# Kernel optimization log

Measured on AMD Instinct MI355X. Metric: run time of the kernel, lower is better.

Reference implementation:

```python
import jax, jax.numpy as jnp
import numpy as np

# Model constants (from source: model_dim=1024, head_dim=128, num_heads=8)
L = 8          # num layers (reduced from 16 for tractable reference memory)
T = 2048       # packed tokens, B == 1 (varlen)
DIM = 1024
NH = 8
NKV = 4        # GQA kv heads
HD = 128
KVD = NKV * HD
BLOCK = 128
WS = 3
WIN = WS * BLOCK           # sliding-window size for 'S' layers
ATTN_SCALE = 0.12
PATTERN = 'SSSL'
GATE_CH = 32
EPS = 1.1920929e-07        # torch F.rms_norm default eps = finfo(fp32).eps


def rms_norm(x):
    return x * jax.lax.rsqrt(jnp.mean(x * x, axis=-1, keepdims=True) + EPS)


def apply_rotary(x, cos, sin):
    # x: [T, H, HD]; cos/sin: [T, 1, HD//2]
    d = x.shape[-1] // 2
    x1, x2 = x[..., :d], x[..., d:]
    return jnp.concatenate([x1 * cos + x2 * sin, -x1 * sin + x2 * cos], axis=-1)


def has_ve(layer_idx, n_layer):
    return layer_idx % 2 == (n_layer - 1) % 2


def setup_inputs() -> dict:
    key = jax.random.key(0)
    ks = jax.random.split(key, 9)
    x = jax.random.normal(ks[0], (1, T, DIM), jnp.float32)
    ve = jax.random.normal(ks[1], (L, T, KVD), jnp.float32)
    s = DIM ** -0.5
    Wq = jax.random.normal(ks[2], (L, DIM, NH * HD), jnp.float32) * s
    Wk = jax.random.normal(ks[3], (L, DIM, KVD), jnp.float32) * s
    Wv = jax.random.normal(ks[4], (L, DIM, KVD), jnp.float32) * s
    Wo = jax.random.normal(ks[5], (L, NH * HD, DIM), jnp.float32) * (NH * HD) ** -0.5
    Wgate = jax.random.normal(ks[6], (L, GATE_CH, NKV), jnp.float32) * GATE_CH ** -0.5
    Wfc = jax.random.normal(ks[7], (L, DIM, 4 * DIM), jnp.float32) * s
    Wproj = jax.random.normal(ks[8], (L, 4 * DIM, DIM), jnp.float32) * (4 * DIM) ** -0.5
    # RoPE tables (absolute positions of the packed batch, as in the source)
    inv_freq = 1.0 / (10000.0 ** (jnp.arange(HD // 2, dtype=jnp.float32) / (HD // 2)))
    ang = jnp.arange(T, dtype=jnp.float32)[:, None] * inv_freq[None, :]
    cos = jnp.cos(ang)[:, None, :]
    sin = jnp.sin(ang)[:, None, :]
    # cu_seqlens: 4 packed documents of 512 tokens
    seqlens = jnp.array([0, 512, 1024, 1536, 2048], dtype=jnp.int32)
    return dict(x=x, ve=ve, Wq=Wq, Wk=Wk, Wv=Wv, Wo=Wo, Wgate=Wgate,
                Wfc=Wfc, Wproj=Wproj, cos=cos, sin=sin, seqlens=seqlens)


def reference(x, ve, Wq, Wk, Wv, Wo, Wgate, Wfc, Wproj, cos, sin, seqlens):
    h = x[0]  # [T, DIM], B == 1 (varlen packing)
    pos = jnp.arange(T)
    doc = jnp.searchsorted(seqlens, pos, side='right') - 1
    diff = pos[:, None] - pos[None, :]
    base = (diff >= 0) & (doc[:, None] == doc[None, :])   # causal within doc
    mask_S = base & (diff <= WIN)                         # sliding window
    neg = jnp.float32(-1e30)
    rep = NH // NKV
    for l in range(L):
        xn = rms_norm(h)
        q = (xn @ Wq[l]).reshape(T, NH, HD)
        k = (xn @ Wk[l]).reshape(T, NKV, HD)
        v = (xn @ Wv[l]).reshape(T, NKV, HD)
        if has_ve(l, L):
            gate = 2.0 * jax.nn.sigmoid(xn[:, :GATE_CH] @ Wgate[l])  # [T, NKV]
            v = v + gate[:, :, None] * ve[l].reshape(T, NKV, HD)
        q = rms_norm(apply_rotary(q, cos, sin))
        k = rms_norm(apply_rotary(k, cos, sin))
        k = jnp.repeat(k, rep, axis=1)   # GQA -> full heads
        v2 = jnp.repeat(v, rep, axis=1)
        scores = jnp.einsum('thd,shd->hts', q, k) * ATTN_SCALE  # [NH, T, T]
        mask = mask_S if PATTERN[l % len(PATTERN)] == 'S' else base
        scores = jnp.where(mask[None], scores, neg)
        p = jax.nn.softmax(scores, axis=-1)
        y = jnp.einsum('hts,shd->thd', p, v2).reshape(T, NH * HD)
        h = h + y @ Wo[l]
        m = jnp.square(jax.nn.relu(rms_norm(h) @ Wfc[l]))  # relu(x)^2 MLP
        h = h + m @ Wproj[l]
    return h[None]
```

## Files before the change

kernel.cpp:

```cpp
#include <hip/hip_runtime.h>
#include <hip/hip_bf16.h>
#include <cstdint>
#include <cstddef>

#define TT     2048
#define DMODEL 1024
#define NHQ    8
#define HD     128
#define KVD    512
#define WIN    384
#define EPSF   1.1920929e-07f
#define SCALE  0.12f

typedef __attribute__((ext_vector_type(8))) short bf16x8;
typedef __attribute__((ext_vector_type(4))) float f32x4;

#define WAITV(N)  asm volatile("s_waitcnt vmcnt(" #N ")" ::: "memory")

__device__ __forceinline__ float b2f(unsigned short u) {
    unsigned int i = ((unsigned int)u) << 16; float f; __builtin_memcpy(&f, &i, 4); return f;
}
__device__ __forceinline__ unsigned short f2b(float f) {
    unsigned int i; __builtin_memcpy(&i, &f, 4);
    unsigned int r = (i + 0x7fffu + ((i >> 16) & 1u)) >> 16;
    return (unsigned short)r;
}

__device__ __forceinline__ void gl_lds16(const unsigned short* g, unsigned short* l) {
    __builtin_amdgcn_global_load_lds(
        (const __attribute__((address_space(1))) unsigned int*)g,
        (__attribute__((address_space(3))) unsigned int*)l, 16, 0, 0);
}

__global__ __launch_bounds__(256)
void convT_k(const float* __restrict__ Wq, const float* __restrict__ Wk,
             const float* __restrict__ Wv, const float* __restrict__ Wo,
             const float* __restrict__ Wfc, const float* __restrict__ Wproj,
             unsigned short* __restrict__ Bqkv, unsigned short* __restrict__ Bo,
             unsigned short* __restrict__ Bfc, unsigned short* __restrict__ Bproj)
{
    __shared__ float lt[64][65];
    const int bid = blockIdx.x, tid = threadIdx.x, l = blockIdx.y;

    const float* W; unsigned short* Wt; int K, N, t, nbase;
    if (bid < 256)        { W = Wq    + (size_t)l * 1024 * 1024; Wt = Bqkv  + (size_t)l * 2048 * 1024; K = 1024; N = 1024; t = bid;        nbase = 0;    }
    else if (bid < 384)   { W = Wk    + (size_t)l * 1024 * 512;  Wt = Bqkv  + (size_t)l * 2048 * 1024; K = 1024; N = 512;  t = bid - 256;  nbase = 1024; }
    else if (bid < 512)   { W = Wv    + (size_t)l * 1024 * 512;  Wt = Bqkv  + (size_t)l * 2048 * 1024; K = 1024; N = 512;  t = bid - 384;  nbase = 1536; }
    else if (bid < 768)   { W = Wo    + (size_t)l * 1024 * 1024; Wt = Bo    + (size_t)l * 1024 * 1024; K = 1024; N = 1024; t = bid - 512;  nbase = 0;    }
    else if (bid < 1792)  { W = Wfc   + (size_t)l * 1024 * 4096; Wt = Bfc   + (size_t)l * 4096 * 1024; K = 1024; N = 4096; t = bid - 768;  nbase = 0;    }
    else                  { W = Wproj + (size_t)l * 4096 * 1024; Wt = Bproj + (size_t)l * 1024 * 4096; K = 4096; N = 1024; t = bid - 1792; nbase = 0;    }

    const int ktiles = K >> 6;
    const int k0 = (t % ktiles) * 64, n0 = (t / ktiles) * 64;

    #pragma unroll
    for (int i = 0; i < 4; ++i) {
        int k = (tid >> 4) + i * 16;
        int col4 = (tid & 15) * 4;
        float4 v = *(const float4*)(W + (size_t)(k0 + k) * N + n0 + col4);
        lt[col4 + 0][k] = v.x;
        lt[col4 + 1][k] = v.y;
        lt[col4 + 2][k] = v.z;
        lt[col4 + 3][k] = v.w;
    }
    __syncthreads();
    #pragma unroll
    for (int i = 0; i < 2; ++i) {
        int idx = tid + i * 256;
        int n = idx >> 3, kc = (idx & 7) * 8;
        unsigned short o[8];
        #pragma unroll
        for (int j = 0; j < 8; ++j) o[j] = f2b(lt[n][kc + j]);
        *(uint4*)(Wt + (size_t)(nbase + n0 + n) * K + k0 + kc) = *(const uint4*)o;
    }
}

template<int EPI>
__global__ __launch_bounds__(256, 2)
void gemm4(const unsigned short* __restrict__ A, const unsigned short* __restrict__ Bt,
           float* __restrict__ Cf, unsigned short* __restrict__ Cb,
           int K, int ksplit, int Ntot)
{
    __shared__ unsigned short As[2 * 128 * 64];
    __shared__ unsigned short Bs[2 * 128 * 64];
    const int BUF = 128 * 64;
    const int tid = threadIdx.x, lane = tid & 63, wv = tid >> 6;

    const int gx = gridDim.x;
    const int nwg = gx * gridDim.y;
    const int ihw = blockIdx.y * gx + blockIdx.x;
    const int q = nwg >> 3, r = nwg & 7;
    const int xcd = ihw & 7, pos = ihw >> 3;
    const int lg = (xcd < r) ? xcd * (q + 1) + pos
                             : r * (q + 1) + (xcd - r) * q + pos;
    const int m0 = (lg % gx) * 128, n0 = (lg / gx) * 128;

    const int kbeg = blockIdx.z * ksplit;
    const int NT = ksplit >> 6;

    const int wr = (wv >> 1) * 64, wc = (wv & 1) * 64;
    const int l15 = lane & 15, g = lane >> 4;
    const int srow = lane >> 3;
    const int sxor = (((lane & 7) ^ srow) << 3);

    const unsigned short* gA0 = A  + (size_t)(m0 + wv * 32 + srow) * K + sxor;
    const unsigned short* gB0 = Bt + (size_t)(n0 + wv * 32 + srow) * K + sxor;

    auto stage = [&](int t) {
        const int b = t & 1;
        const size_t k = (size_t)kbeg + ((size_t)t << 6);
        unsigned short* la = As + b * BUF + (wv * 32) * 64;
        unsigned short* lb = Bs + b * BUF + (wv * 32) * 64;
        #pragma unroll
        for (int c = 0; c < 4; ++c) {
            gl_lds16(gA0 + (size_t)(c * 8) * K + k, la + c * 8 * 64);
            gl_lds16(gB0 + (size_t)(c * 8) * K + k, lb + c * 8 * 64);
        }
    };

    f32x4 acc[4][4] = {};

    stage(0);
    for (int t = 0; t < NT; ++t) {
        if (t + 1 < NT) { stage(t + 1); WAITV(8); }
        else            { WAITV(0); }
        __builtin_amdgcn_s_barrier();

        const unsigned short* Ac = As + (t & 1) * BUF;
        const unsigned short* Bc = Bs + (t & 1) * BUF;
        bf16x8 af[4][2], bfv[4][2];
        #pragma unroll
        for (int mi = 0; mi < 4; ++mi) {
            const int row = wr + mi * 16 + l15, x = row & 7;
            #pragma unroll
            for (int kk = 0; kk < 2; ++kk)
                af[mi][kk] = *(const bf16x8*)(Ac + row * 64 + (((kk * 4 + g) ^ x) << 3));
        }
        #pragma unroll
        for (int ni = 0; ni < 4; ++ni) {
            const int row = wc + ni * 16 + l15, x = row & 7;
            #pragma unroll
            for (int kk = 0; kk < 2; ++kk)
                bfv[ni][kk] = *(const bf16x8*)(Bc + row * 64 + (((kk * 4 + g) ^ x) << 3));
        }
        __builtin_amdgcn_s_setprio(1);
        #pragma unroll
        for (int kk = 0; kk < 2; ++kk)
            #pragma unroll
            for (int mi = 0; mi < 4; ++mi)
                #pragma unroll
                for (int ni = 0; ni < 4; ++ni)
                    acc[mi][ni] = __builtin_amdgcn_mfma_f32_16x16x32_bf16(af[mi][kk], bfv[ni][kk], acc[mi][ni], 0, 0, 0);
        __builtin_amdgcn_s_setprio(0);
        __builtin_amdgcn_s_barrier();
    }

    const int lr4 = (lane >> 4) * 4;
    float* Cz = Cf + (size_t)blockIdx.z * TT * Ntot;
    #pragma unroll
    for (int mi = 0; mi < 4; ++mi)
        #pragma unroll
        for (int ni = 0; ni < 4; ++ni)
            #pragma unroll
            for (int r2 = 0; r2 < 4; ++r2) {
                int row = m0 + wr + mi * 16 + lr4 + r2;
                int col = n0 + wc + ni * 16 + l15;
                size_t idx = (size_t)row * Ntot + col;
                float v = acc[mi][ni][r2];
                if (EPI == 0) Cz[idx] = v;
                else {
                    float z = v > 0.f ? v * v : 0.f;
                    Cb[idx] = f2b(z);
                }
            }
}

__global__ __launch_bounds__(256)
void rmsnormF_k(float* __restrict__ h, const float* __restrict__ part, int nz,
                unsigned short* __restrict__ xn)
{
    const int t = blockIdx.x, tid = threadIdx.x;
    const size_t idx = (size_t)t * (DMODEL / 4) + tid;
    float4 v = ((const float4*)h)[idx];
    for (int z = 0; z < nz; ++z) {
        float4 p = ((const float4*)part)[idx + (size_t)z * (TT * DMODEL / 4)];
        v.x += p.x; v.y += p.y; v.z += p.z; v.w += p.w;
    }
    if (nz > 0) ((float4*)h)[idx] = v;

    float ss = v.x*v.x + v.y*v.y + v.z*v.z + v.w*v.w;
    #pragma unroll
    for (int m = 1; m < 64; m <<= 1) ss += __shfl_xor(ss, m);
    __shared__ float red[4];
    if ((tid & 63) == 0) red[tid >> 6] = ss;
    __syncthreads();
    float tot = red[0] + red[1] + red[2] + red[3];
    float rs = rsqrtf(tot * (1.f / DMODEL) + EPSF);
    unsigned short o[4] = { f2b(v.x*rs), f2b(v.y*rs), f2b(v.z*rs), f2b(v.w*rs) };
    *(ushort4*)(xn + (size_t)t * DMODEL + tid * 4) = *(const ushort4*)o;
}

__global__ __launch_bounds__(256)
void reduce_add_k(float* __restrict__ h, const float* __restrict__ part, int nz)
{
    const int i = blockIdx.x * 256 + threadIdx.x;
    float4 a = ((const float4*)part)[i];
    for (int z = 1; z < nz; ++z) {
        float4 p = ((const float4*)part)[i + (size_t)z * (TT * DMODEL / 4)];
        a.x += p.x; a.y += p.y; a.z += p.z; a.w += p.w;
    }
    float4 hv = ((float4*)h)[i];
    hv.x += a.x; hv.y += a.y; hv.z += a.z; hv.w += a.w;
    ((float4*)h)[i] = hv;
}

__global__ __launch_bounds__(256)
void post_qkv_k(const float* __restrict__ qkv, const unsigned short* __restrict__ xn,
                const float* __restrict__ cosb, const float* __restrict__ sinb,
                const float* __restrict__ Wgate, const float* __restrict__ vel, int hasve,
                unsigned short* __restrict__ qn, unsigned short* __restrict__ kn,
                unsigned short* __restrict__ vrow)
{
    const size_t S2 = (size_t)TT * 2048;
    const int t = blockIdx.x, tid = threadIdx.x;
    __shared__ float cs[64], sn[64], gate[4];
    if (tid < 64) { cs[tid] = cosb[t * 64 + tid]; sn[tid] = sinb[t * 64 + tid]; }
    if (hasve && tid >= 64 && tid < 68) {
        int g = tid - 64; float a = 0.f;
        for (int c = 0; c < 32; ++c) a += b2f(xn[(size_t)t * DMODEL + c]) * Wgate[c * 4 + g];
        gate[g] = 2.f / (1.f + __expf(-a));
    }
    __syncthreads();
    if (tid < 96) {
        const int hid = tid >> 3, sub = tid & 7;
        const float* src; unsigned short* dst;
        if (hid < 8) { src = qkv + (size_t)t * 2048 + hid * 128;              dst = qn + (size_t)t * 1024 + hid * 128; }
        else         { src = qkv + (size_t)t * 2048 + 1024 + (hid - 8) * 128; dst = kn + (size_t)t * 512 + (hid - 8) * 128; }
        float o1[8], o2[8], ssum = 0.f;
        #pragma unroll
        for (int j = 0; j < 8; ++j) {
            int jj = sub * 8 + j;
            float x1 = src[jj] + src[jj + S2];
            float x2 = src[jj + 64] + src[jj + 64 + S2];
            float c = cs[jj], s = sn[jj];
            o1[j] = x1 * c + x2 * s;
            o2[j] = -x1 * s + x2 * c;
            ssum += o1[j]*o1[j] + o2[j]*o2[j];
        }
        ssum += __shfl_xor(ssum, 1); ssum += __shfl_xor(ssum, 2); ssum += __shfl_xor(ssum, 4);
        float rs = rsqrtf(ssum * (1.f / HD) + EPSF);
        #pragma unroll
        for (int j = 0; j < 8; ++j) {
            int jj = sub * 8 + j;
            dst[jj]      = f2b(o1[j] * rs);
            dst[jj + 64] = f2b(o2[j] * rs);
        }
    }
    {
        int d0 = tid * 2;
        #pragma unroll
        for (int j = 0; j < 2; ++j) {
            int d = d0 + j;
            size_t off = (size_t)t * 2048 + 1536 + d;
            float vv = qkv[off] + qkv[off + S2];
            if (hasve) vv += gate[d >> 7] * vel[(size_t)t * KVD + d];
            vrow[(size_t)t * KVD + d] = f2b(vv);
        }
    }
}

__global__ __launch_bounds__(256)
void vtrans_k(const unsigned short* __restrict__ vrow, unsigned short* __restrict__ vt)
{
    __shared__ unsigned short lt[64][72];
    const int t0 = blockIdx.x * 64, c0 = blockIdx.y * 64, tid = threadIdx.x;
    #pragma unroll
    for (int i = 0; i < 2; ++i) {
        int r = (tid >> 3) + i * 32;
        int c = (tid & 7) * 8;
        bf16x8 v = *(const bf16x8*)(vrow + (size_t)(t0 + r) * KVD + c0 + c);
        #pragma unroll
        for (int j = 0; j < 8; ++j) lt[c + j][r] = ((unsigned short*)&v)[j];
    }
    __syncthreads();
    #pragma unroll
    for (int i = 0; i < 2; ++i) {
        int r = (tid >> 3) + i * 32;
        int c = (tid & 7) * 8;
        *(bf16x8*)(vt + (size_t)(c0 + r) * TT + t0 + c) = *(const bf16x8*)(&lt[r][c]);
    }
}

__global__ __launch_bounds__(256)
void attn_k(const unsigned short* __restrict__ qn, const unsigned short* __restrict__ kn,
            const unsigned short* __restrict__ vt, unsigned short* __restrict__ y,
            const int* __restrict__ seqlens, int isS)
{
    __shared__ unsigned short Plds[4][16][40];
    const int tid = threadIdx.x, w = tid >> 6, lane = tid & 63;
    const int h = blockIdx.y, hkv = h >> 1;
    const int qr = (blockIdx.x * 4 + w) * 16;
    const int s1 = seqlens[1], s2 = seqlens[2], s3 = seqlens[3];
    const int l15 = lane & 15, lhi = lane >> 4;

    bf16x8 qf[4];
    #pragma unroll
    for (int kk = 0; kk < 4; ++kk)
        qf[kk] = *(const bf16x8*)(qn + (size_t)(qr + l15) * 1024 + h * HD + kk * 32 + lhi * 8);

    int drow[4];
    #pragma unroll
    for (int r = 0; r < 4; ++r) {
        int row = qr + lhi * 4 + r;
        drow[r] = (row >= s1) + (row >= s2) + (row >= s3);
    }
    int dq = (qr >= s1) + (qr >= s2) + (qr >= s3);
    int dstart = dq == 0 ? 0 : (dq == 1 ? s1 : (dq == 2 ? s2 : s3));
    int smin = dstart;
    if (isS) { int wlo = qr - WIN; if (wlo > smin) smin = wlo; }
    if (smin < 0) smin = 0;
    const int smax = qr + 16;

    f32x4 acc[8] = {};
    float mrow[4] = { -1e30f, -1e30f, -1e30f, -1e30f };
    float lrow[4] = { 0.f, 0.f, 0.f, 0.f };

    for (int s0 = smin & ~31; s0 < smax; s0 += 32) {
        float sv[2][4];
        #pragma unroll
        for (int nb = 0; nb < 2; ++nb) {
            f32x4 S = {};
            int scol = s0 + nb * 16 + l15;
            int scl = scol < TT ? scol : TT - 1;
            #pragma unroll
            for (int kk = 0; kk < 4; ++kk) {
                bf16x8 kf = *(const bf16x8*)(kn + (size_t)scl * KVD + hkv * HD + kk * 32 + lhi * 8);
                S = __builtin_amdgcn_mfma_f32_16x16x32_bf16(qf[kk], kf, S, 0, 0, 0);
            }
            int dcol = (scol >= s1) + (scol >= s2) + (scol >= s3);
            #pragma unroll
            for (int r = 0; r < 4; ++r) {
                int row = qr + lhi * 4 + r;
                bool valid = (scol <= row) && (dcol == drow[r]) && (!isS || (row - scol) <= WIN);
                sv[nb][r] = valid ? S[r] * SCALE : -1e30f;
            }
        }
        #pragma unroll
        for (int r = 0; r < 4; ++r) {
            float pm = fmaxf(sv[0][r], sv[1][r]);
            pm = fmaxf(pm, __shfl_xor(pm, 1));
            pm = fmaxf(pm, __shfl_xor(pm, 2));
            pm = fmaxf(pm, __shfl_xor(pm, 4));
            pm = fmaxf(pm, __shfl_xor(pm, 8));
            float mnew = fmaxf(mrow[r], pm);
            float scl2 = __expf(mrow[r] - mnew);
            float p0 = __expf(sv[0][r] - mnew);
            float p1 = __expf(sv[1][r] - mnew);
            float ps = p0 + p1;
            ps += __shfl_xor(ps, 1); ps += __shfl_xor(ps, 2);
            ps += __shfl_xor(ps, 4); ps += __shfl_xor(ps, 8);
            lrow[r] = lrow[r] * scl2 + ps;
            mrow[r] = mnew;
            #pragma unroll
            for (int nb = 0; nb < 8; ++nb) acc[nb][r] *= scl2;
            Plds[w][lhi * 4 + r][l15]      = f2b(p0);
            Plds[w][lhi * 4 + r][16 + l15] = f2b(p1);
        }
        bf16x8 pf = *(const bf16x8*)(&Plds[w][l15][lhi * 8]);
        #pragma unroll
        for (int nb = 0; nb < 8; ++nb) {
            bf16x8 vf = *(const bf16x8*)(vt + (size_t)(hkv * HD + nb * 16 + l15) * TT + s0 + lhi * 8);
            acc[nb] = __builtin_amdgcn_mfma_f32_16x16x32_bf16(pf, vf, acc[nb], 0, 0, 0);
        }
    }
    #pragma unroll
    for (int r = 0; r < 4; ++r) {
        float inv = 1.f / lrow[r];
        int row = qr + lhi * 4 + r;
        #pragma unroll
        for (int nb = 0; nb < 8; ++nb)
            y[(size_t)row * 1024 + h * HD + nb * 16 + l15] = f2b(acc[nb][r] * inv);
    }
}

extern "C" void kernel_launch(void* const* d_in, const int* in_sizes, int n_in,
                              void* d_out, int out_size, void* d_ws, size_t ws_size,
                              hipStream_t stream)
{
    const float* x       = (const float*)d_in[0];
    const float* ve      = (const float*)d_in[1];
    const float* Wq      = (const float*)d_in[2];
    const float* Wk      = (const float*)d_in[3];
    const float* Wv      = (const float*)d_in[4];
    const float* Wo      = (const float*)d_in[5];
    const float* Wgate   = (const float*)d_in[6];
    const float* Wfc     = (const float*)d_in[7];
    const float* Wproj   = (const float*)d_in[8];
    const float* cosb    = (const float*)d_in[9];
    const float* sinb    = (const float*)d_in[10];
    const int*   seqlens = (const int*)d_in[11];

    float* h = (float*)d_out;
    char* ws = (char*)d_ws;
    unsigned short* xn    = (unsigned short*)(ws);
    unsigned short* qn    = (unsigned short*)(ws + (4ull  << 20));
    unsigned short* kn    = (unsigned short*)(ws + (8ull  << 20));
    unsigned short* vrow  = (unsigned short*)(ws + (10ull << 20));
    unsigned short* vt    = (unsigned short*)(ws + (12ull << 20));
    unsigned short* yb    = (unsigned short*)(ws + (14ull << 20));
    unsigned short* mb    = (unsigned short*)(ws + (18ull << 20));
    float*          part  = (float*)(ws + (34ull << 20));
    unsigned short* Bqkv  = (unsigned short*)(ws + (66ull  << 20));
    unsigned short* Bo    = (unsigned short*)(ws + (98ull  << 20));
    unsigned short* Bfc   = (unsigned short*)(ws + (114ull << 20));
    unsigned short* Bproj = (unsigned short*)(ws + (178ull << 20));

    hipMemcpyAsync(h, x, (size_t)TT * DMODEL * sizeof(float), hipMemcpyDeviceToDevice, stream);

    convT_k<<<dim3(2816, 8), 256, 0, stream>>>(Wq, Wk, Wv, Wo, Wfc, Wproj,
                                               Bqkv, Bo, Bfc, Bproj);

    for (int l = 0; l < 8; ++l) {
        int hasve = (l % 2) == 1;
        int isS   = (l % 4) != 3;

        rmsnormF_k<<<TT, 256, 0, stream>>>(h, part, l == 0 ? 0 : 4, xn);

        gemm4<0><<<dim3(16, 16, 2), 256, 0, stream>>>(xn, Bqkv + (size_t)l * 2048 * 1024,
                                                      part, nullptr, 1024, 512, 2048);

        post_qkv_k<<<TT, 256, 0, stream>>>(part, xn, cosb, sinb,
            Wgate + (size_t)l * 128, ve + (size_t)l * TT * KVD, hasve, qn, kn, vrow);

        vtrans_k<<<dim3(32, 8), 256, 0, stream>>>(vrow, vt);

        attn_k<<<dim3(32, 8), 256, 0, stream>>>(qn, kn, vt, yb, seqlens, isS);

        gemm4<0><<<dim3(16, 8, 2), 256, 0, stream>>>(yb, Bo + (size_t)l * 1024 * 1024,
                                                     part, nullptr, 1024, 512, 1024);

        rmsnormF_k<<<TT, 256, 0, stream>>>(h, part, 2, xn);

        gemm4<2><<<dim3(16, 32, 1), 256, 0, stream>>>(xn, Bfc + (size_t)l * 4096 * 1024,
                                                      nullptr, mb, 1024, 1024, 4096);

        gemm4<0><<<dim3(16, 8, 4), 256, 0, stream>>>(mb, Bproj + (size_t)l * 1024 * 4096,
                                                     part, nullptr, 4096, 1024, 1024);
    }

    reduce_add_k<<<2048, 256, 0, stream>>>(h, part, 4);
}
```

Measured before the change: 1.465 ms.

## Store split-K GEMM partials in bf16 and restructure attention to transposed S via shuffles

```diff
diff --git a/kernel.cpp b/kernel.cpp
--- a/kernel.cpp
+++ b/kernel.cpp
@@ -78,8 +78,7 @@
 template<int EPI>
 __global__ __launch_bounds__(256, 2)
 void gemm4(const unsigned short* __restrict__ A, const unsigned short* __restrict__ Bt,
-           float* __restrict__ Cf, unsigned short* __restrict__ Cb,
-           int K, int ksplit, int Ntot)
+           unsigned short* __restrict__ Cp, int K, int ksplit, int Ntot)
 {
     __shared__ unsigned short As[2 * 128 * 64];
     __shared__ unsigned short Bs[2 * 128 * 64];
@@ -156,7 +155,7 @@
     }
 
     const int lr4 = (lane >> 4) * 4;
-    float* Cz = Cf + (size_t)blockIdx.z * TT * Ntot;
+    unsigned short* Cz = Cp + (size_t)blockIdx.z * TT * Ntot;
     #pragma unroll
     for (int mi = 0; mi < 4; ++mi)
         #pragma unroll
@@ -167,24 +166,24 @@
                 int col = n0 + wc + ni * 16 + l15;
                 size_t idx = (size_t)row * Ntot + col;
                 float v = acc[mi][ni][r2];
-                if (EPI == 0) Cz[idx] = v;
+                if (EPI == 0) Cz[idx] = f2b(v);
                 else {
                     float z = v > 0.f ? v * v : 0.f;
-                    Cb[idx] = f2b(z);
+                    Cz[idx] = f2b(z);
                 }
             }
 }
 
 __global__ __launch_bounds__(256)
-void rmsnormF_k(float* __restrict__ h, const float* __restrict__ part, int nz,
+void rmsnormF_k(float* __restrict__ h, const unsigned short* __restrict__ part, int nz,
                 unsigned short* __restrict__ xn)
 {
     const int t = blockIdx.x, tid = threadIdx.x;
     const size_t idx = (size_t)t * (DMODEL / 4) + tid;
     float4 v = ((const float4*)h)[idx];
     for (int z = 0; z < nz; ++z) {
-        float4 p = ((const float4*)part)[idx + (size_t)z * (TT * DMODEL / 4)];
-        v.x += p.x; v.y += p.y; v.z += p.z; v.w += p.w;
+        ushort4 p = ((const ushort4*)part)[idx + (size_t)z * (TT * DMODEL / 4)];
+        v.x += b2f(p.x); v.y += b2f(p.y); v.z += b2f(p.z); v.w += b2f(p.w);
     }
     if (nz > 0) ((float4*)h)[idx] = v;
 
@@ -201,21 +200,19 @@
 }
 
 __global__ __launch_bounds__(256)
-void reduce_add_k(float* __restrict__ h, const float* __restrict__ part, int nz)
+void reduce_add_k(float* __restrict__ h, const unsigned short* __restrict__ part, int nz)
 {
     const int i = blockIdx.x * 256 + threadIdx.x;
-    float4 a = ((const float4*)part)[i];
-    for (int z = 1; z < nz; ++z) {
-        float4 p = ((const float4*)part)[i + (size_t)z * (TT * DMODEL / 4)];
-        a.x += p.x; a.y += p.y; a.z += p.z; a.w += p.w;
-    }
     float4 hv = ((float4*)h)[i];
-    hv.x += a.x; hv.y += a.y; hv.z += a.z; hv.w += a.w;
+    for (int z = 0; z < nz; ++z) {
+        ushort4 p = ((const ushort4*)part)[i + (size_t)z * (TT * DMODEL / 4)];
+        hv.x += b2f(p.x); hv.y += b2f(p.y); hv.z += b2f(p.z); hv.w += b2f(p.w);
+    }
     ((float4*)h)[i] = hv;
 }
 
 __global__ __launch_bounds__(256)
-void post_qkv_k(const float* __restrict__ qkv, const unsigned short* __restrict__ xn,
+void post_qkv_k(const unsigned short* __restrict__ qkv, const unsigned short* __restrict__ xn,
                 const float* __restrict__ cosb, const float* __restrict__ sinb,
                 const float* __restrict__ Wgate, const float* __restrict__ vel, int hasve,
                 unsigned short* __restrict__ qn, unsigned short* __restrict__ kn,
@@ -233,15 +230,15 @@
     __syncthreads();
     if (tid < 96) {
         const int hid = tid >> 3, sub = tid & 7;
-        const float* src; unsigned short* dst;
+        const unsigned short* src; unsigned short* dst;
         if (hid < 8) { src = qkv + (size_t)t * 2048 + hid * 128;              dst = qn + (size_t)t * 1024 + hid * 128; }
         else         { src = qkv + (size_t)t * 2048 + 1024 + (hid - 8) * 128; dst = kn + (size_t)t * 512 + (hid - 8) * 128; }
         float o1[8], o2[8], ssum = 0.f;
         #pragma unroll
         for (int j = 0; j < 8; ++j) {
             int jj = sub * 8 + j;
-            float x1 = src[jj] + src[jj + S2];
-            float x2 = src[jj + 64] + src[jj + 64 + S2];
+            float x1 = b2f(src[jj])      + b2f(src[jj + S2]);
+            float x2 = b2f(src[jj + 64]) + b2f(src[jj + 64 + S2]);
             float c = cs[jj], s = sn[jj];
             o1[j] = x1 * c + x2 * s;
             o2[j] = -x1 * s + x2 * c;
@@ -262,7 +259,7 @@
         for (int j = 0; j < 2; ++j) {
             int d = d0 + j;
             size_t off = (size_t)t * 2048 + 1536 + d;
-            float vv = qkv[off] + qkv[off + S2];
+            float vv = b2f(qkv[off]) + b2f(qkv[off + S2]);
             if (hasve) vv += gate[d >> 7] * vel[(size_t)t * KVD + d];
             vrow[(size_t)t * KVD + d] = f2b(vv);
         }
@@ -296,24 +293,21 @@
             const unsigned short* __restrict__ vt, unsigned short* __restrict__ y,
             const int* __restrict__ seqlens, int isS)
 {
-    __shared__ unsigned short Plds[4][16][40];
+    __shared__ float Ot[4][16][132];
     const int tid = threadIdx.x, w = tid >> 6, lane = tid & 63;
     const int h = blockIdx.y, hkv = h >> 1;
     const int qr = (blockIdx.x * 4 + w) * 16;
     const int s1 = seqlens[1], s2 = seqlens[2], s3 = seqlens[3];
-    const int l15 = lane & 15, lhi = lane >> 4;
+    const int l15 = lane & 15, g = lane >> 4;
 
     bf16x8 qf[4];
     #pragma unroll
     for (int kk = 0; kk < 4; ++kk)
-        qf[kk] = *(const bf16x8*)(qn + (size_t)(qr + l15) * 1024 + h * HD + kk * 32 + lhi * 8);
-
-    int drow[4];
-    #pragma unroll
-    for (int r = 0; r < 4; ++r) {
-        int row = qr + lhi * 4 + r;
-        drow[r] = (row >= s1) + (row >= s2) + (row >= s3);
-    }
+        qf[kk] = *(const bf16x8*)(qn + (size_t)(qr + l15) * 1024 + h * HD + kk * 32 + g * 8);
+
+    const int row = qr + l15;
+    const int drow = (row >= s1) + (row >= s2) + (row >= s3);
+
     int dq = (qr >= s1) + (qr >= s2) + (qr >= s3);
     int dstart = dq == 0 ? 0 : (dq == 1 ? s1 : (dq == 2 ? s2 : s3));
     int smin = dstart;
@@ -322,64 +316,93 @@
     const int smax = qr + 16;
 
     f32x4 acc[8] = {};
-    float mrow[4] = { -1e30f, -1e30f, -1e30f, -1e30f };
-    float lrow[4] = { 0.f, 0.f, 0.f, 0.f };
+    float mrow = -1e30f, lrow = 0.f;
 
     for (int s0 = smin & ~31; s0 < smax; s0 += 32) {
+        f32x4 S[2] = {};
+        __builtin_amdgcn_s_setprio(1);
+        #pragma unroll
+        for (int nb = 0; nb < 2; ++nb) {
+            int srow = s0 + nb * 16 + l15;
+            #pragma unroll
+            for (int kk = 0; kk < 4; ++kk) {
+                bf16x8 kf = *(const bf16x8*)(kn + (size_t)srow * KVD + hkv * HD + kk * 32 + g * 8);
+                S[nb] = __builtin_amdgcn_mfma_f32_16x16x32_bf16(kf, qf[kk], S[nb], 0, 0, 0);
+            }
+        }
+        __builtin_amdgcn_s_setprio(0);
+
         float sv[2][4];
         #pragma unroll
-        for (int nb = 0; nb < 2; ++nb) {
-            f32x4 S = {};
-            int scol = s0 + nb * 16 + l15;
-            int scl = scol < TT ? scol : TT - 1;
-            #pragma unroll
-            for (int kk = 0; kk < 4; ++kk) {
-                bf16x8 kf = *(const bf16x8*)(kn + (size_t)scl * KVD + hkv * HD + kk * 32 + lhi * 8);
-                S = __builtin_amdgcn_mfma_f32_16x16x32_bf16(qf[kk], kf, S, 0, 0, 0);
+        for (int nb = 0; nb < 2; ++nb)
+            #pragma unroll
+            for (int r = 0; r < 4; ++r) {
+                int s = s0 + nb * 16 + 4 * g + r;
+                int dcol = (s >= s1) + (s >= s2) + (s >= s3);
+                bool valid = (s <= row) && (dcol == drow) && (!isS || (row - s) <= WIN);
+                sv[nb][r] = valid ? S[nb][r] * SCALE : -1e30f;
             }
-            int dcol = (scol >= s1) + (scol >= s2) + (scol >= s3);
+
+        float pm = sv[0][0];
+        #pragma unroll
+        for (int r = 1; r < 4; ++r) pm = fmaxf(pm, sv[0][r]);
+        #pragma unroll
+        for (int r = 0; r < 4; ++r) pm = fmaxf(pm, sv[1][r]);
+        pm = fmaxf(pm, __shfl_xor(pm, 16));
+        pm = fmaxf(pm, __shfl_xor(pm, 32));
+        float mnew = fmaxf(mrow, pm);
+        float scl2 = __expf(mrow - mnew);
+        float p0[4], p1[4], ps = 0.f;
+        #pragma unroll
+        for (int r = 0; r < 4; ++r) {
+            p0[r] = __expf(sv[0][r] - mnew);
+            p1[r] = __expf(sv[1][r] - mnew);
+            ps += p0[r] + p1[r];
+        }
+        ps += __shfl_xor(ps, 16);
+        ps += __shfl_xor(ps, 32);
+        lrow = lrow * scl2 + ps;
+        mrow = mnew;
+        #pragma unroll
+        for (int nb2 = 0; nb2 < 8; ++nb2) acc[nb2] *= scl2;
+
+        unsigned short pt[8];
+        const int base = l15 + ((g & 1) << 5);
+        #pragma unroll
+        for (int jh = 0; jh < 2; ++jh)
             #pragma unroll
             for (int r = 0; r < 4; ++r) {
-                int row = qr + lhi * 4 + r;
-                bool valid = (scol <= row) && (dcol == drow[r]) && (!isS || (row - scol) <= WIN);
-                sv[nb][r] = valid ? S[r] * SCALE : -1e30f;
+                float ta = __shfl(p0[r], base + 16 * jh);
+                float tb = __shfl(p1[r], base + 16 * jh);
+                pt[jh * 4 + r] = f2b(g >= 2 ? tb : ta);
             }
-        }
-        #pragma unroll
-        for (int r = 0; r < 4; ++r) {
-            float pm = fmaxf(sv[0][r], sv[1][r]);
-            pm = fmaxf(pm, __shfl_xor(pm, 1));
-            pm = fmaxf(pm, __shfl_xor(pm, 2));
-            pm = fmaxf(pm, __shfl_xor(pm, 4));
-            pm = fmaxf(pm, __shfl_xor(pm, 8));
-            float mnew = fmaxf(mrow[r], pm);
-            float scl2 = __expf(mrow[r] - mnew);
-            float p0 = __expf(sv[0][r] - mnew);
-            float p1 = __expf(sv[1][r] - mnew);
-            float ps = p0 + p1;
-            ps += __shfl_xor(ps, 1); ps += __shfl_xor(ps, 2);
-            ps += __shfl_xor(ps, 4); ps += __shfl_xor(ps, 8);
-            lrow[r] = lrow[r] * scl2 + ps;
-            mrow[r] = mnew;
-            #pragma unroll
-            for (int nb = 0; nb < 8; ++nb) acc[nb][r] *= scl2;
-            Plds[w][lhi * 4 + r][l15]      = f2b(p0);
-            Plds[w][lhi * 4 + r][16 + l15] = f2b(p1);
-        }
-        bf16x8 pf = *(const bf16x8*)(&Plds[w][l15][lhi * 8]);
-        #pragma unroll
-        for (int nb = 0; nb < 8; ++nb) {
-            bf16x8 vf = *(const bf16x8*)(vt + (size_t)(hkv * HD + nb * 16 + l15) * TT + s0 + lhi * 8);
-            acc[nb] = __builtin_amdgcn_mfma_f32_16x16x32_bf16(pf, vf, acc[nb], 0, 0, 0);
-        }
-    }
-    #pragma unroll
-    for (int r = 0; r < 4; ++r) {
-        float inv = 1.f / lrow[r];
-        int row = qr + lhi * 4 + r;
-        #pragma unroll
-        for (int nb = 0; nb < 8; ++nb)
-            y[(size_t)row * 1024 + h * HD + nb * 16 + l15] = f2b(acc[nb][r] * inv);
+        bf16x8 pf;
+        #pragma unroll
+        for (int j = 0; j < 8; ++j) ((unsigned short*)&pf)[j] = pt[j];
+
+        __builtin_amdgcn_s_setprio(1);
+        #pragma unroll
+        for (int nb2 = 0; nb2 < 8; ++nb2) {
+            bf16x8 vf = *(const bf16x8*)(vt + (size_t)(hkv * HD + nb2 * 16 + l15) * TT + s0 + g * 8);
+            acc[nb2] = __builtin_amdgcn_mfma_f32_16x16x32_bf16(vf, pf, acc[nb2], 0, 0, 0);
+        }
+        __builtin_amdgcn_s_setprio(0);
+    }
+
+    const float inv = 1.f / lrow;
+    #pragma unroll
+    for (int nb2 = 0; nb2 < 8; ++nb2)
+        #pragma unroll
+        for (int r = 0; r < 4; ++r)
+            Ot[w][l15][nb2 * 16 + 4 * g + r] = acc[nb2][r] * inv;
+    __syncthreads();
+    const int qo = lane >> 2, dblk = (lane & 3) * 32;
+    #pragma unroll
+    for (int i4 = 0; i4 < 4; ++i4) {
+        unsigned short ob[8];
+        #pragma unroll
+        for (int j = 0; j < 8; ++j) ob[j] = f2b(Ot[w][qo][dblk + i4 * 8 + j]);
+        *(uint4*)(y + (size_t)(qr + qo) * 1024 + h * HD + dblk + i4 * 8) = *(const uint4*)ob;
     }
 }
 
@@ -409,11 +432,11 @@
     unsigned short* vt    = (unsigned short*)(ws + (12ull << 20));
     unsigned short* yb    = (unsigned short*)(ws + (14ull << 20));
     unsigned short* mb    = (unsigned short*)(ws + (18ull << 20));
-    float*          part  = (float*)(ws + (34ull << 20));
-    unsigned short* Bqkv  = (unsigned short*)(ws + (66ull  << 20));
-    unsigned short* Bo    = (unsigned short*)(ws + (98ull  << 20));
-    unsigned short* Bfc   = (unsigned short*)(ws + (114ull << 20));
-    unsigned short* Bproj = (unsigned short*)(ws + (178ull << 20));
+    unsigned short* part  = (unsigned short*)(ws + (34ull << 20));
+    unsigned short* Bqkv  = (unsigned short*)(ws + (50ull  << 20));
+    unsigned short* Bo    = (unsigned short*)(ws + (82ull  << 20));
+    unsigned short* Bfc   = (unsigned short*)(ws + (98ull  << 20));
+    unsigned short* Bproj = (unsigned short*)(ws + (162ull << 20));
 
     hipMemcpyAsync(h, x, (size_t)TT * DMODEL * sizeof(float), hipMemcpyDeviceToDevice, stream);
 
@@ -427,7 +450,7 @@
         rmsnormF_k<<<TT, 256, 0, stream>>>(h, part, l == 0 ? 0 : 4, xn);
 
         gemm4<0><<<dim3(16, 16, 2), 256, 0, stream>>>(xn, Bqkv + (size_t)l * 2048 * 1024,
-                                                      part, nullptr, 1024, 512, 2048);
+                                                      part, 1024, 512, 2048);
 
         post_qkv_k<<<TT, 256, 0, stream>>>(part, xn, cosb, sinb,
             Wgate + (size_t)l * 128, ve + (size_t)l * TT * KVD, hasve, qn, kn, vrow);
@@ -437,15 +460,15 @@
         attn_k<<<dim3(32, 8), 256, 0, stream>>>(qn, kn, vt, yb, seqlens, isS);
 
         gemm4<0><<<dim3(16, 8, 2), 256, 0, stream>>>(yb, Bo + (size_t)l * 1024 * 1024,
-                                                     part, nullptr, 1024, 512, 1024);
+                                                     part, 1024, 512, 1024);
 
         rmsnormF_k<<<TT, 256, 0, stream>>>(h, part, 2, xn);
 
         gemm4<2><<<dim3(16, 32, 1), 256, 0, stream>>>(xn, Bfc + (size_t)l * 4096 * 1024,
-                                                      nullptr, mb, 1024, 1024, 4096);
+                                                      mb, 1024, 1024, 4096);
 
         gemm4<0><<<dim3(16, 8, 4), 256, 0, stream>>>(mb, Bproj + (size_t)l * 1024 * 4096,
-                                                     part, nullptr, 4096, 1024, 1024);
+                                                     part, 4096, 1024, 1024);
     }
 
     reduce_add_k<<<2048, 256, 0, stream>>>(h, part, 4);
```

Result: faster. 1.404 ms (-4.2%).
